# Performance work log

Measured on AMD Instinct MI355X. Metric: run time of the kernel, lower is better.

The kernel has to match this reference:

```python
import jax, jax.numpy as jnp
import numpy as np

N = 100000  # nodes
E = 500000  # directed edges (before self-loops)

def _glorot(key, fi, fo):
    s = np.sqrt(6.0 / (fi + fo)).astype(np.float32)
    return jax.random.uniform(key, (fi, fo), jnp.float32, -s, s)

def setup_inputs() -> dict:
    key = jax.random.key(0)
    ks = jax.random.split(key, 6)
    x = jax.random.normal(ks[0], (N, 128), jnp.float32)
    edge_index = jax.random.randint(ks[1], (2, E), 0, N, dtype=jnp.int64)
    return {
        "x": x,
        "edge_index": edge_index,
        "W1": _glorot(ks[2], 128, 512), "b1": jnp.zeros((512,), jnp.float32),
        "W2": _glorot(ks[3], 512, 768), "b2": jnp.zeros((768,), jnp.float32),
        "W3": _glorot(ks[4], 768, 512), "b3": jnp.zeros((512,), jnp.float32),
        "W4": _glorot(ks[5], 512, 128), "b4": jnp.zeros((128,), jnp.float32),
    }

def reference(x, edge_index, W1, b1, W2, b2, W3, b3, W4, b4):
    # PyG GCNConv: add self-loops, deg from dst index, sym-normalized scatter-add.
    loops = jnp.arange(N, dtype=edge_index.dtype)
    src = jnp.concatenate([edge_index[0], loops])  # [E+N]
    dst = jnp.concatenate([edge_index[1], loops])  # [E+N]
    deg = jax.ops.segment_sum(jnp.ones_like(dst, jnp.float32), dst, num_segments=N)
    dinv = jax.lax.rsqrt(deg)  # deg >= 1 thanks to self-loops
    norm = (dinv[src] * dinv[dst])[:, None]  # [E+N, 1]

    def gcn_conv(h, W, b):
        hw = h @ W                                  # [N, Fout] dense linear
        msg = norm * hw[src]                        # [E+N, Fout] gather + scale
        return jax.ops.segment_sum(msg, dst, num_segments=N) + b

    h = jax.nn.gelu(gcn_conv(x, W1, b1), approximate=False)
    h = jax.nn.gelu(gcn_conv(h, W2, b2), approximate=False)
    h = jax.nn.gelu(gcn_conv(h, W3, b3), approximate=False)
    return gcn_conv(h, W4, b4)
```

## Files before the change

kernel.cpp:

```cpp
#include <hip/hip_runtime.h>

typedef short bf16x8 __attribute__((ext_vector_type(8)));
typedef float f32x4 __attribute__((ext_vector_type(4)));

__device__ __forceinline__ float b2f(unsigned short u) {
  union { unsigned int i; float f; } x; x.i = ((unsigned int)u) << 16; return x.f;
}
__device__ __forceinline__ unsigned short f2b(float f) {
  union { float f; unsigned int u; } x; x.f = f;
  unsigned int r = (x.u + 0x7FFFu + ((x.u >> 16) & 1u)) >> 16;
  return (unsigned short)r;
}
__device__ __forceinline__ float gelu_f(float v) {
  return 0.5f * v * (1.0f + erff(v * 0.70710678118654752440f));
}


__global__ void count_kernel(const int* __restrict__ ei, int E, int* __restrict__ cnt) {
  int e = blockIdx.x * 256 + threadIdx.x;
  if (e < E) atomicAdd(&cnt[ei[E + e]], 1);
}

__global__ void dinv_kernel(const int* __restrict__ cnt, float* __restrict__ dinv, int Nn) {
  int n = blockIdx.x * 256 + threadIdx.x;
  if (n < Nn) dinv[n] = rsqrtf((float)cnt[n] + 1.0f);
}


__global__ __launch_bounds__(256) void scanA_kernel(const int* __restrict__ cnt,
                                                    int* __restrict__ bsum, int Nn) {
  __shared__ int red[256];
  const int t = threadIdx.x;
  const int base = blockIdx.x * 512 + t * 2;
  int a = (base < Nn) ? cnt[base] : 0;
  int b = (base + 1 < Nn) ? cnt[base + 1] : 0;
  red[t] = a + b;
  __syncthreads();
  for (int d = 128; d > 0; d >>= 1) {
    if (t < d) red[t] += red[t + d];
    __syncthreads();
  }
  if (t == 0) bsum[blockIdx.x] = red[0];
}

__global__ __launch_bounds__(256) void scanB_kernel(const int* __restrict__ bsum,
                                                    int* __restrict__ boff,
                                                    int* __restrict__ rowstart,
                                                    int NBLK, int Nn) {
  __shared__ int sh[256];
  const int t = threadIdx.x;
  sh[t] = (t < NBLK) ? bsum[t] : 0;
  __syncthreads();
  for (int d = 1; d < 256; d <<= 1) {
    int x = sh[t];
    int add = (t >= d) ? sh[t - d] : 0;
    __syncthreads();
    sh[t] = x + add;
    __syncthreads();
  }
  if (t < NBLK) boff[t] = (t == 0) ? 0 : sh[t - 1];
  if (t == NBLK - 1) rowstart[Nn] = sh[t];
}

__global__ __launch_bounds__(256) void scanC_kernel(const int* __restrict__ cnt,
                                                    const int* __restrict__ boff,
                                                    int* __restrict__ rowstart,
                                                    int* __restrict__ cursor, int Nn) {
  __shared__ int sh[256];
  const int t = threadIdx.x;
  const int base = blockIdx.x * 512 + t * 2;
  int a = (base < Nn) ? cnt[base] : 0;
  int b = (base + 1 < Nn) ? cnt[base + 1] : 0;
  sh[t] = a + b;
  __syncthreads();
  for (int d = 1; d < 256; d <<= 1) {
    int x = sh[t];
    int add = (t >= d) ? sh[t - d] : 0;
    __syncthreads();
    sh[t] = x + add;
    __syncthreads();
  }
  const int off = boff[blockIdx.x] + ((t == 0) ? 0 : sh[t - 1]);
  if (base < Nn) { rowstart[base] = off; cursor[base] = off; }
  if (base + 1 < Nn) { rowstart[base + 1] = off + a; cursor[base + 1] = off + a; }
}

__global__ void fill_kernel(const int* __restrict__ ei, int E, const float* __restrict__ dinv,
                            int* __restrict__ cursor, int* __restrict__ ssrc,
                            float* __restrict__ snorm) {
  int e = blockIdx.x * 256 + threadIdx.x;
  if (e < E) {
    int s = ei[e], d = ei[E + e];
    int pos = atomicAdd(&cursor[d], 1);
    ssrc[pos] = s;
    snorm[pos] = dinv[s] * dinv[d];
  }
}

__global__ void wtrans_kernel(const float* __restrict__ W, unsigned short* __restrict__ WT,
                              int K, int N) {
  int i = blockIdx.x * 256 + threadIdx.x;
  if (i < K * N) {
    int n = i / K, k = i - n * K;
    WT[i] = f2b(W[k * N + n]);
  }
}


template <int F, bool INF32, bool OUTF32, bool HASBIAS, bool DOGELU>
__global__ __launch_bounds__(256) void agg_kernel(
    const int* __restrict__ rowstart, const int* __restrict__ ssrc,
    const float* __restrict__ snorm, const float* __restrict__ dinv,
    const void* __restrict__ inv, const float* __restrict__ bias,
    void* __restrict__ outv, int Nn) {
  constexpr int V = F / 64;
  const int lane = threadIdx.x & 63;
  const int node = blockIdx.x * 4 + (threadIdx.x >> 6);
  if (node >= Nn) return;
  const int base = lane * V;
  float acc[V];
  {
    float w = dinv[node]; w = w * w;
    if constexpr (INF32) {
      const float* in = (const float*)inv + (size_t)node * F + base;
      if constexpr (V == 2) {
        float2 v = *(const float2*)in; acc[0] = w * v.x; acc[1] = w * v.y;
      } else {
        float4 v0 = *(const float4*)in; float4 v1 = *(const float4*)(in + 4);
        acc[0] = w * v0.x; acc[1] = w * v0.y; acc[2] = w * v0.z; acc[3] = w * v0.w;
        acc[4] = w * v1.x; acc[5] = w * v1.y; acc[6] = w * v1.z; acc[7] = w * v1.w;
      }
    } else {
      const unsigned short* in = (const unsigned short*)inv + (size_t)node * F + base;
      if constexpr (V == 2) {
        unsigned int v = *(const unsigned int*)in;
        acc[0] = w * b2f(v & 0xffffu); acc[1] = w * b2f(v >> 16);
      } else {
        bf16x8 v = *(const bf16x8*)in;
#pragma unroll
        for (int i = 0; i < 8; ++i) acc[i] = w * b2f((unsigned short)v[i]);
      }
    }
  }
  const int e0 = rowstart[node], e1 = rowstart[node + 1];
  for (int e = e0; e < e1; ++e) {
    const int s = ssrc[e];
    const float w = snorm[e];
    if constexpr (INF32) {
      const float* in = (const float*)inv + (size_t)s * F + base;
      if constexpr (V == 2) {
        float2 v = *(const float2*)in; acc[0] += w * v.x; acc[1] += w * v.y;
      } else {
        float4 v0 = *(const float4*)in; float4 v1 = *(const float4*)(in + 4);
        acc[0] += w * v0.x; acc[1] += w * v0.y; acc[2] += w * v0.z; acc[3] += w * v0.w;
        acc[4] += w * v1.x; acc[5] += w * v1.y; acc[6] += w * v1.z; acc[7] += w * v1.w;
      }
    } else {
      const unsigned short* in = (const unsigned short*)inv + (size_t)s * F + base;
      if constexpr (V == 2) {
        unsigned int v = *(const unsigned int*)in;
        acc[0] += w * b2f(v & 0xffffu); acc[1] += w * b2f(v >> 16);
      } else {
        bf16x8 v = *(const bf16x8*)in;
#pragma unroll
        for (int i = 0; i < 8; ++i) acc[i] += w * b2f((unsigned short)v[i]);
      }
    }
  }
  if constexpr (HASBIAS) {
#pragma unroll
    for (int i = 0; i < V; ++i) acc[i] += bias[base + i];
  }
  if constexpr (DOGELU) {
#pragma unroll
    for (int i = 0; i < V; ++i) acc[i] = gelu_f(acc[i]);
  }
  if constexpr (OUTF32) {
    float* out = (float*)outv + (size_t)node * F + base;
#pragma unroll
    for (int i = 0; i < V; ++i) out[i] = acc[i];
  } else {
    unsigned short* out = (unsigned short*)outv + (size_t)node * F + base;
    if constexpr (V == 2) {
      unsigned int pack = (unsigned int)f2b(acc[0]) | ((unsigned int)f2b(acc[1]) << 16);
      *(unsigned int*)out = pack;
    } else {
      bf16x8 o;
#pragma unroll
      for (int i = 0; i < 8; ++i) o[i] = (short)f2b(acc[i]);
      *(bf16x8*)out = o;
    }
  }
}


template <bool HASBIAS, bool DOGELU>
__global__ __launch_bounds__(256) void gemm_bt(
    const unsigned short* __restrict__ A, const unsigned short* __restrict__ BT,
    const float* __restrict__ bias, unsigned short* __restrict__ C,
    int N, int K, int NT) {
  __shared__ alignas(16) unsigned short Asl[128 * 32];
  __shared__ alignas(16) unsigned short Bsl[128 * 32];
  const int tid = threadIdx.x;
  const int lane = tid & 63;
  const int wid = tid >> 6;

  const int G = gridDim.x;
  const int q = G >> 3, r = G & 7;
  const int xcd = blockIdx.x & 7, ii = blockIdx.x >> 3;
  const int w = (xcd < r ? xcd * (q + 1) : r * (q + 1) + (xcd - r) * q) + ii;
  const int bx = w / NT;
  const int by = w - bx * NT;

  const size_t brow = (size_t)bx * 128;
  const size_t bcol = (size_t)by * 128;
  const int wr = (wid >> 1) * 64;
  const int wc = (wid & 1) * 64;
  const int rr = lane & 15, rg = lane >> 4;
  f32x4 acc[4][4] = {};
  const int KT = K >> 5;
  for (int kt = 0; kt < KT; ++kt) {
    const int kb = kt << 5;
#pragma unroll
    for (int rsub = 0; rsub < 2; ++rsub) {
      const int c = tid + rsub * 256;
      const int arow = c >> 2;
      const int jlog = (c & 3) ^ ((arow >> 1) & 3);
      const unsigned short* gA = A + (brow + arow) * K + kb + jlog * 8;
      __builtin_amdgcn_global_load_lds((const __attribute__((address_space(1))) void*)gA,
                                       (__attribute__((address_space(3))) void*)(&Asl[c * 8]),
                                       16, 0, 0);
      const unsigned short* gB = BT + (bcol + arow) * K + kb + jlog * 8;
      __builtin_amdgcn_global_load_lds((const __attribute__((address_space(1))) void*)gB,
                                       (__attribute__((address_space(3))) void*)(&Bsl[c * 8]),
                                       16, 0, 0);
    }
    __syncthreads();
    bf16x8 af[4], bfr[4];
#pragma unroll
    for (int m = 0; m < 4; ++m) {
      const int R = wr + m * 16 + rr;
      af[m] = *(const bf16x8*)(&Asl[R * 32 + ((rg ^ ((R >> 1) & 3)) * 8)]);
    }
#pragma unroll
    for (int n = 0; n < 4; ++n) {
      const int R = wc + n * 16 + rr;
      bfr[n] = *(const bf16x8*)(&Bsl[R * 32 + ((rg ^ ((R >> 1) & 3)) * 8)]);
    }
#pragma unroll
    for (int m = 0; m < 4; ++m)
#pragma unroll
      for (int n = 0; n < 4; ++n)
        acc[m][n] = __builtin_amdgcn_mfma_f32_16x16x32_bf16(af[m], bfr[n], acc[m][n], 0, 0, 0);
    __syncthreads();
  }
#pragma unroll
  for (int m = 0; m < 4; ++m) {
    size_t row0 = brow + wr + m * 16 + rg * 4;
#pragma unroll
    for (int n = 0; n < 4; ++n) {
      size_t col = bcol + wc + n * 16 + rr;
      float bv = 0.0f;
      if constexpr (HASBIAS) bv = bias[col];
#pragma unroll
      for (int r2 = 0; r2 < 4; ++r2) {
        float v = acc[m][n][r2] + bv;
        if constexpr (DOGELU) v = gelu_f(v);
        C[(row0 + r2) * N + col] = f2b(v);
      }
    }
  }
}


extern "C" void kernel_launch(void* const* d_in, const int* in_sizes, int n_in,
                              void* d_out, int out_size, void* d_ws, size_t ws_size,
                              hipStream_t stream) {
  const float* x = (const float*)d_in[0];
  const int* ei = (const int*)d_in[1];
  const float* W1 = (const float*)d_in[2]; const float* b1 = (const float*)d_in[3];
  const float* W2 = (const float*)d_in[4]; const float* b2 = (const float*)d_in[5];
  const float* W3 = (const float*)d_in[6]; const float* b3 = (const float*)d_in[7];
  const float* W4 = (const float*)d_in[8]; const float* b4 = (const float*)d_in[9];

  const int Nn = in_sizes[0] / 128;
  const int E = in_sizes[1] / 2;
  const int Mpad = (Nn + 127) & ~127;

  char* p = (char*)d_ws;
  auto alloc = [&](size_t bytes) {
    char* r = p;
    p += (bytes + 255) & ~(size_t)255;
    return r;
  };
  float* dinv = (float*)alloc((size_t)Nn * 4);
  int* cnt = (int*)alloc((size_t)Nn * 4);
  int* rowstart = (int*)alloc((size_t)(Nn + 1) * 4);
  int* cursor = (int*)alloc((size_t)Nn * 4);
  int* ssrc = (int*)alloc((size_t)E * 4);
  float* snorm = (float*)alloc((size_t)E * 4);
  int* bsum = (int*)alloc((size_t)256 * 4);
  int* boff = (int*)alloc((size_t)256 * 4);
  unsigned short* WT1 = (unsigned short*)alloc((size_t)512 * 128 * 2);
  unsigned short* WT2 = (unsigned short*)alloc((size_t)768 * 512 * 2);
  unsigned short* WT3 = (unsigned short*)alloc((size_t)512 * 768 * 2);
  unsigned short* WT4 = (unsigned short*)alloc((size_t)128 * 512 * 2);
  unsigned short* bufA = (unsigned short*)alloc((size_t)Mpad * 512 * 2);
  unsigned short* bufB = (unsigned short*)alloc((size_t)Mpad * 768 * 2);

  const int EB = (E + 255) / 256;
  const int NB = (Nn + 255) / 256;
  const int AGGB = (Nn + 3) / 4;
  const int MT = Mpad / 128;
  const int NSCAN = (Nn + 511) / 512;

  hipMemsetAsync(cnt, 0, (size_t)Nn * 4, stream);
  count_kernel<<<EB, 256, 0, stream>>>(ei, E, cnt);
  dinv_kernel<<<NB, 256, 0, stream>>>(cnt, dinv, Nn);
  scanA_kernel<<<NSCAN, 256, 0, stream>>>(cnt, bsum, Nn);
  scanB_kernel<<<1, 256, 0, stream>>>(bsum, boff, rowstart, NSCAN, Nn);
  scanC_kernel<<<NSCAN, 256, 0, stream>>>(cnt, boff, rowstart, cursor, Nn);
  fill_kernel<<<EB, 256, 0, stream>>>(ei, E, dinv, cursor, ssrc, snorm);
  wtrans_kernel<<<(128 * 512 + 255) / 256, 256, 0, stream>>>(W1, WT1, 128, 512);
  wtrans_kernel<<<(512 * 768 + 255) / 256, 256, 0, stream>>>(W2, WT2, 512, 768);
  wtrans_kernel<<<(768 * 512 + 255) / 256, 256, 0, stream>>>(W3, WT3, 768, 512);
  wtrans_kernel<<<(512 * 128 + 255) / 256, 256, 0, stream>>>(W4, WT4, 512, 128);

  agg_kernel<128, true, false, false, false><<<AGGB, 256, 0, stream>>>(
      rowstart, ssrc, snorm, dinv, x, nullptr, bufA, Nn);
  gemm_bt<true, true><<<MT * 4, 256, 0, stream>>>(bufA, WT1, b1, bufB, 512, 128, 4);

  agg_kernel<512, false, false, false, false><<<AGGB, 256, 0, stream>>>(
      rowstart, ssrc, snorm, dinv, bufB, nullptr, bufA, Nn);
  gemm_bt<true, true><<<MT * 6, 256, 0, stream>>>(bufA, WT2, b2, bufB, 768, 512, 6);

  gemm_bt<false, false><<<MT * 4, 256, 0, stream>>>(bufB, WT3, nullptr, bufA, 512, 768, 4);
  agg_kernel<512, false, false, true, true><<<AGGB, 256, 0, stream>>>(
      rowstart, ssrc, snorm, dinv, bufA, b3, bufB, Nn);

  gemm_bt<false, false><<<MT * 1, 256, 0, stream>>>(bufB, WT4, nullptr, bufA, 128, 512, 1);
  agg_kernel<128, false, true, true, false><<<AGGB, 256, 0, stream>>>(
      rowstart, ssrc, snorm, dinv, bufA, b4, d_out, Nn);
}
```

Baseline: 759.7 us.

## Add 256x256 double-buffered LDS-DMA GEMM for the three wide layers

Adds a new GEMM kernel with 512 threads and a 256x256 output tile over 64-wide K steps. Operands are double-buffered in LDS via global_load_lds with an XOR swizzle, and each wave computes a 128x64 sub-tile with 16x16x32 bf16 MFMAs. It replaces the 128x128 gemm_bt for layers 1-3 to raise data reuse per tile and overlap loads with compute. Mpad is rounded up to 256 to fit the new tiles. The cost is 128 KB of LDS per block and a large accumulator register footprint, which may limit occupancy despite launch_bounds(512,2). Fewer blocks on a 256-CU part also risks tail imbalance.

```diff
diff --git a/kernel.cpp b/kernel.cpp
--- a/kernel.cpp
+++ b/kernel.cpp
@@ -195,6 +195,98 @@
 
 
 template <bool HASBIAS, bool DOGELU>
+__global__ __launch_bounds__(512, 2) void gemm256(
+    const unsigned short* __restrict__ A, const unsigned short* __restrict__ BT,
+    const float* __restrict__ bias, unsigned short* __restrict__ C,
+    int N, int K, int NT) {
+  __shared__ alignas(16) unsigned short As[2][256 * 64];
+  __shared__ alignas(16) unsigned short Bs[2][256 * 64];
+  const int tid = threadIdx.x;
+  const int lane = tid & 63;
+  const int wid = tid >> 6;
+  const int wr = wid >> 2;
+  const int wc = wid & 3;
+  const int rr = lane & 15, rg = lane >> 4;
+
+  const int G = gridDim.x;
+  const int q = G >> 3, r = G & 7;
+  const int xcd = blockIdx.x & 7, ii = blockIdx.x >> 3;
+  const int w = (xcd < r ? xcd * (q + 1) : r * (q + 1) + (xcd - r) * q) + ii;
+  const int bx = w / NT;
+  const int by = w - bx * NT;
+  const size_t brow = (size_t)bx * 256;
+  const size_t bcol = (size_t)by * 256;
+
+  const int nt = K >> 6;
+
+  auto stage = [&](int t) {
+    const int kb = t << 6;
+    const int buf = t & 1;
+#pragma unroll
+    for (int j = 0; j < 4; ++j) {
+      const int s = tid + 512 * j;
+      const int row = s >> 3;
+      const int lslot = (s & 7) ^ (row & 7);
+      const unsigned short* gA = A + (brow + row) * K + kb + lslot * 8;
+      __builtin_amdgcn_global_load_lds((const __attribute__((address_space(1))) void*)gA,
+          (__attribute__((address_space(3))) void*)(&As[buf][s * 8]), 16, 0, 0);
+      const unsigned short* gB = BT + (bcol + row) * K + kb + lslot * 8;
+      __builtin_amdgcn_global_load_lds((const __attribute__((address_space(1))) void*)gB,
+          (__attribute__((address_space(3))) void*)(&Bs[buf][s * 8]), 16, 0, 0);
+    }
+  };
+
+  f32x4 acc[8][4] = {};
+  stage(0);
+  __syncthreads();
+  for (int t = 0; t < nt; ++t) {
+    if (t + 1 < nt) stage(t + 1);
+    const int buf = t & 1;
+    bf16x8 bq[2][4];
+#pragma unroll
+    for (int kk = 0; kk < 2; ++kk)
+#pragma unroll
+      for (int nb = 0; nb < 4; ++nb) {
+        const int R = wc * 64 + nb * 16 + rr;
+        const int ps = (kk * 4 + rg) ^ (R & 7);
+        bq[kk][nb] = *(const bf16x8*)(&Bs[buf][R * 64 + ps * 8]);
+      }
+#pragma unroll
+    for (int mb = 0; mb < 8; ++mb) {
+      const int R = wr * 128 + mb * 16 + rr;
+      const int ps0 = rg ^ (R & 7);
+      const int ps1 = (4 + rg) ^ (R & 7);
+      bf16x8 a0 = *(const bf16x8*)(&As[buf][R * 64 + ps0 * 8]);
+      bf16x8 a1 = *(const bf16x8*)(&As[buf][R * 64 + ps1 * 8]);
+#pragma unroll
+      for (int nb = 0; nb < 4; ++nb)
+        acc[mb][nb] = __builtin_amdgcn_mfma_f32_16x16x32_bf16(a0, bq[0][nb], acc[mb][nb], 0, 0, 0);
+#pragma unroll
+      for (int nb = 0; nb < 4; ++nb)
+        acc[mb][nb] = __builtin_amdgcn_mfma_f32_16x16x32_bf16(a1, bq[1][nb], acc[mb][nb], 0, 0, 0);
+    }
+    __syncthreads();
+  }
+#pragma unroll
+  for (int mb = 0; mb < 8; ++mb) {
+    size_t row0 = brow + wr * 128 + mb * 16 + rg * 4;
+#pragma unroll
+    for (int nb = 0; nb < 4; ++nb) {
+      size_t col = bcol + wc * 64 + nb * 16 + rr;
+      float bv = 0.0f;
+      if constexpr (HASBIAS) bv = bias[col];
+#pragma unroll
+      for (int r2 = 0; r2 < 4; ++r2) {
+        float v = acc[mb][nb][r2] + bv;
+        if constexpr (DOGELU) v = gelu_f(v);
+        C[(row0 + r2) * N + col] = f2b(v);
+      }
+    }
+  }
+}
+
+
+template <bool HASBIAS, bool DOGELU>
 __global__ __launch_bounds__(256) void gemm_bt(
     const unsigned short* __restrict__ A, const unsigned short* __restrict__ BT,
     const float* __restrict__ bias, unsigned short* __restrict__ C,
@@ -285,7 +377,7 @@
 
   const int Nn = in_sizes[0] / 128;
   const int E = in_sizes[1] / 2;
-  const int Mpad = (Nn + 127) & ~127;
+  const int Mpad = (Nn + 255) & ~255;
 
   char* p = (char*)d_ws;
   auto alloc = [&](size_t bytes) {
@@ -311,7 +403,8 @@
   const int EB = (E + 255) / 256;
   const int NB = (Nn + 255) / 256;
   const int AGGB = (Nn + 3) / 4;
-  const int MT = Mpad / 128;
+  const int MT128 = Mpad / 128;
+  const int MT256 = Mpad / 256;
   const int NSCAN = (Nn + 511) / 512;
 
   hipMemsetAsync(cnt, 0, (size_t)Nn * 4, stream);
@@ -328,17 +421,17 @@
 
   agg_kernel<128, true, false, false, false><<<AGGB, 256, 0, stream>>>(
       rowstart, ssrc, snorm, dinv, x, nullptr, bufA, Nn);
-  gemm_bt<true, true><<<MT * 4, 256, 0, stream>>>(bufA, WT1, b1, bufB, 512, 128, 4);
+  gemm256<true, true><<<MT256 * 2, 512, 0, stream>>>(bufA, WT1, b1, bufB, 512, 128, 2);
 
   agg_kernel<512, false, false, false, false><<<AGGB, 256, 0, stream>>>(
       rowstart, ssrc, snorm, dinv, bufB, nullptr, bufA, Nn);
-  gemm_bt<true, true><<<MT * 6, 256, 0, stream>>>(bufA, WT2, b2, bufB, 768, 512, 6);
-
-  gemm_bt<false, false><<<MT * 4, 256, 0, stream>>>(bufB, WT3, nullptr, bufA, 512, 768, 4);
+  gemm256<true, true><<<MT256 * 3, 512, 0, stream>>>(bufA, WT2, b2, bufB, 768, 512, 3);
+
+  gemm256<false, false><<<MT256 * 2, 512, 0, stream>>>(bufB, WT3, nullptr, bufA, 512, 768, 2);
   agg_kernel<512, false, false, true, true><<<AGGB, 256, 0, stream>>>(
       rowstart, ssrc, snorm, dinv, bufA, b3, bufB, Nn);
 
-  gemm_bt<false, false><<<MT * 1, 256, 0, stream>>>(bufB, WT4, nullptr, bufA, 128, 512, 1);
+  gemm_bt<false, false><<<MT128 * 1, 256, 0, stream>>>(bufB, WT4, nullptr, bufA, 128, 512, 1);
   agg_kernel<128, false, true, true, false><<<AGGB, 256, 0, stream>>>(
       rowstart, ssrc, snorm, dinv, bufA, b4, d_out, Nn);
 }
```

Measured after the change: 767.5 us. About the same (+1.0%).
